# Performance work log

Hardware: AMD Instinct MI355X
Metric: run time of the kernel (lower is better)

## Reference

```python
import jax, jax.numpy as jnp
import numpy as np


def setup_inputs() -> dict:
    key = jax.random.key(0)
    k1, k2, k3, k4 = jax.random.split(key, 4)
    B, H, W = 16, 256, 256
    CF = 128  # FeatureDA channels
    return {
        "infeat": jax.random.normal(k1, (B, 2, H, W), jnp.float32),
        "labelTpesudo": jax.random.uniform(k2, (B, 1, H, W), jnp.float32),
        "labelT": jax.random.uniform(k3, (B, 1, H, W), jnp.float32),
        "FeatureDA": jax.random.normal(k4, (B, CF, H, W), jnp.float32),
        "k": 2,
        "size": 32,
    }


def _gather_points(x, bi, yy, xx):
    # x: [B, C, H, W]; bi/yy/xx: [n_cls, B, k] -> [n_cls, B, k, C]
    return x.transpose(0, 2, 3, 1)[bi, yy, xx]


def reference(infeat, labelTpesudo, labelT, FeatureDA, k, size):
    B, C, H, W = infeat.shape  # C = 2 classes
    maxc = H - 1  # orisize - 1
    out = jax.nn.softmax(infeat, axis=1)  # channel softmax (implicit dim=1 for 4D)
    flat = out.reshape(B, C, H * W)
    # torch.topk(k*size*size, sorted=True); only the first k entries are used
    vals, idx = jax.lax.top_k(flat, k * size * size)  # [B, C, k*size*size]
    idx_k = idx[:, :, :k].transpose(1, 0, 2)   # [C, B, k], class-major like the c-loop
    vals_k = vals[:, :, :k].transpose(1, 0, 2)  # [C, B, k]
    # grid_xy: x = flat_index % W, y = flat_index // W
    py = idx_k // W
    px = idx_k % W
    bi = jnp.broadcast_to(jnp.arange(B)[None, :, None], idx_k.shape)
    # each loop iteration gathers a single pixel at (oy[0], ox[0]) = (py, px)
    # (stride=1, padding=0 => max(0, px*1-0) == px)
    classiferT = _gather_points(infeat, bi, py, px).reshape(-1, C)                      # 'ClassiferT'
    patchFeatDA = _gather_points(FeatureDA, bi, py, px).reshape(-1, FeatureDA.shape[1])  # 'patchFeatDA'
    labelTTrue = _gather_points(labelT, bi, py, px).reshape(-1, labelT.shape[1])
    labelpesudo = _gather_points(labelTpesudo, bi, py, px).reshape(-1, labelTpesudo.shape[1])
    provalue = vals_k.reshape(-1, 1)  # values[i, :, j]
    # oxy = [[ox0, ox1], [oy0, oy1]] with hardcoded 32-pixel extent, clamped to orisize-1
    ox = jnp.stack([px, jnp.minimum(px + 32 - 1, maxc)], axis=-1)
    oy = jnp.stack([py, jnp.minimum(py + 32 - 1, maxc)], axis=-1)
    pointXY = jnp.stack([ox, oy], axis=-2).reshape(-1, 2, 2).astype(jnp.int32)
    # concatenation order matches Pixel_select_gen: all unchg (c=0) then chg (c=1)
    return classiferT, patchFeatDA, labelTTrue, labelpesudo, provalue, pointXY
```

## Files before the change

kernel.cpp:

```cpp
#include <hip/hip_runtime.h>
#include <math.h>

static constexpr int Bb   = 16;
static constexpr int Ww   = 256;
static constexpr int HWp  = 256 * 256;
static constexpr int CF   = 128;
static constexpr int Kk   = 2;
static constexpr int SEGS = 8;
static constexpr int SEGLEN = HWp / SEGS;

__device__ __forceinline__ bool better(float v1, int i1, float v2, int i2) {
    return (v1 > v2) || ((v1 == v2) && (i1 < i2));
}

__global__ __launch_bounds__(256) void top2_partial(
    const float* __restrict__ infeat, float* __restrict__ ws_v, int* __restrict__ ws_i)
{
    const int row = blockIdx.x;
    const int seg = blockIdx.y;
    const int b = row >> 1, c = row & 1;
    const float* x0p = infeat + (size_t)(b * 2 + 0) * HWp;
    const float* x1p = infeat + (size_t)(b * 2 + 1) * HWp;
    const int t = threadIdx.x;

    float v0 = -INFINITY, v1 = -INFINITY;
    int   i0 = 0x7fffffff, i1 = 0x7fffffff;

    const int base = seg * SEGLEN + t * 4;
    #pragma unroll
    for (int it = 0; it < SEGLEN / (256 * 4); ++it) {
        const int p = base + it * (256 * 4);
        const float4 a  = *(const float4*)(x0p + p);
        const float4 bb = *(const float4*)(x1p + p);
        const float ax[4] = {a.x, a.y, a.z, a.w};
        const float bx[4] = {bb.x, bb.y, bb.z, bb.w};
        #pragma unroll
        for (int e = 0; e < 4; ++e) {
            const float m  = fmaxf(ax[e], bx[e]);
            const float e0 = expf(ax[e] - m);
            const float e1 = expf(bx[e] - m);
            const float v  = (c == 0 ? e0 : e1) / (e0 + e1);
            const int p2 = p + e;
            if (better(v, p2, v0, i0)) { v1 = v0; i1 = i0; v0 = v; i0 = p2; }
            else if (better(v, p2, v1, i1)) { v1 = v; i1 = p2; }
        }
    }

    __shared__ float sv[256][2];
    __shared__ int   si[256][2];
    sv[t][0] = v0; sv[t][1] = v1; si[t][0] = i0; si[t][1] = i1;
    __syncthreads();
    for (int s = 128; s > 0; s >>= 1) {
        if (t < s) {
            float a0 = sv[t][0], a1 = sv[t][1];
            int  ia0 = si[t][0], ia1 = si[t][1];
            float b0 = sv[t + s][0], b1 = sv[t + s][1];
            int  ib0 = si[t + s][0], ib1 = si[t + s][1];
            float r0, r1; int j0, j1;
            if (better(a0, ia0, b0, ib0)) {
                r0 = a0; j0 = ia0;
                if (better(b0, ib0, a1, ia1)) { r1 = b0; j1 = ib0; } else { r1 = a1; j1 = ia1; }
            } else {
                r0 = b0; j0 = ib0;
                if (better(a0, ia0, b1, ib1)) { r1 = a0; j1 = ia0; } else { r1 = b1; j1 = ib1; }
            }
            sv[t][0] = r0; sv[t][1] = r1; si[t][0] = j0; si[t][1] = j1;
        }
        __syncthreads();
    }
    if (t < 2) {
        ws_v[(row * SEGS + seg) * 2 + t] = sv[0][t];
        ws_i[(row * SEGS + seg) * 2 + t] = si[0][t];
    }
}

__global__ __launch_bounds__(128) void gather_out(
    const float* __restrict__ infeat,
    const float* __restrict__ labelTpesudo,
    const float* __restrict__ labelT,
    const float* __restrict__ FeatureDA,
    const float* __restrict__ ws_v, const int* __restrict__ ws_i,
    float* __restrict__ out)
{
    const int pi = blockIdx.x;
    const int c  = pi / (Bb * Kk);
    const int b  = (pi / Kk) % Bb;
    const int j  = pi % Kk;
    const int row = b * 2 + c;

    __shared__ float s_val;
    __shared__ int   s_idx;
    if (threadIdx.x == 0) {
        float bv0 = -INFINITY, bv1 = -INFINITY;
        int   bi0 = 0x7fffffff, bi1 = 0x7fffffff;
        for (int s2 = 0; s2 < SEGS; ++s2) {
            #pragma unroll
            for (int e = 0; e < 2; ++e) {
                const float v = ws_v[(row * SEGS + s2) * 2 + e];
                const int   i = ws_i[(row * SEGS + s2) * 2 + e];
                if (better(v, i, bv0, bi0)) { bv1 = bv0; bi1 = bi0; bv0 = v; bi0 = i; }
                else if (better(v, i, bv1, bi1)) { bv1 = v; bi1 = i; }
            }
        }
        s_val = (j == 0) ? bv0 : bv1;
        s_idx = (j == 0) ? bi0 : bi1;
    }
    __syncthreads();

    const int   idx = s_idx;
    const float val = s_val;
    const int py = idx >> 8;
    const int px = idx & (Ww - 1);
    const int t = threadIdx.x;

    out[128 + pi * CF + t] = FeatureDA[((size_t)b * CF + t) * HWp + idx];
    if (t < 2) out[pi * 2 + t] = infeat[((size_t)b * 2 + t) * HWp + idx];
    if (t == 0) {
        out[8320 + pi] = labelT[(size_t)b * HWp + idx];
        out[8384 + pi] = labelTpesudo[(size_t)b * HWp + idx];
        out[8448 + pi] = val;
        out[8512 + pi * 4 + 0] = (float)px;
        out[8512 + pi * 4 + 1] = (float)min(px + 31, 255);
        out[8512 + pi * 4 + 2] = (float)py;
        out[8512 + pi * 4 + 3] = (float)min(py + 31, 255);
    }
}

extern "C" void kernel_launch(void* const* d_in, const int* in_sizes, int n_in,
                              void* d_out, int out_size, void* d_ws, size_t ws_size,
                              hipStream_t stream) {
    const float* infeat       = (const float*)d_in[0];
    const float* labelTpesudo = (const float*)d_in[1];
    const float* labelT       = (const float*)d_in[2];
    const float* FeatureDA    = (const float*)d_in[3];
    float* out = (float*)d_out;

    float* ws_v = (float*)d_ws;
    int*   ws_i = (int*)((char*)d_ws + 32 * SEGS * 2 * sizeof(float));

    dim3 g1(32, SEGS);
    top2_partial<<<g1, 256, 0, stream>>>(infeat, ws_v, ws_i);
    gather_out<<<64, 128, 0, stream>>>(infeat, labelTpesudo, labelT, FeatureDA,
                                       ws_v, ws_i, out);
}
```

Baseline: 17.98 us.

## Compute both class top-2s per block and reduce with wave shuffles

```diff
diff --git a/kernel.cpp b/kernel.cpp
--- a/kernel.cpp
+++ b/kernel.cpp
@@ -6,30 +6,47 @@
 static constexpr int HWp  = 256 * 256;
 static constexpr int CF   = 128;
 static constexpr int Kk   = 2;
-static constexpr int SEGS = 8;
+static constexpr int SEGS = 16;
 static constexpr int SEGLEN = HWp / SEGS;
+static constexpr int THREADS = 256;
 
 __device__ __forceinline__ bool better(float v1, int i1, float v2, int i2) {
     return (v1 > v2) || ((v1 == v2) && (i1 < i2));
 }
 
-__global__ __launch_bounds__(256) void top2_partial(
+__device__ __forceinline__ void upd(float v, int p,
+                                    float& v0, int& i0, float& v1, int& i1) {
+    if (better(v, p, v0, i0)) { v1 = v0; i1 = i0; v0 = v; i0 = p; }
+    else if (better(v, p, v1, i1)) { v1 = v; i1 = p; }
+}
+
+__device__ __forceinline__ void merge2(float& a0, int& ia0, float& a1, int& ia1,
+                                       float b0, int ib0, float b1, int ib1) {
+    if (better(b0, ib0, a0, ia0)) {
+        float na1; int nia1;
+        if (better(a0, ia0, b1, ib1)) { na1 = a0; nia1 = ia0; }
+        else                          { na1 = b1; nia1 = ib1; }
+        a0 = b0; ia0 = ib0; a1 = na1; ia1 = nia1;
+    } else if (better(b0, ib0, a1, ia1)) {
+        a1 = b0; ia1 = ib0;
+    }
+}
+
+__global__ __launch_bounds__(THREADS) void top2_partial(
     const float* __restrict__ infeat, float* __restrict__ ws_v, int* __restrict__ ws_i)
 {
-    const int row = blockIdx.x;
+    const int b   = blockIdx.x;
     const int seg = blockIdx.y;
-    const int b = row >> 1, c = row & 1;
-    const float* x0p = infeat + (size_t)(b * 2 + 0) * HWp;
-    const float* x1p = infeat + (size_t)(b * 2 + 1) * HWp;
-    const int t = threadIdx.x;
+    const int t   = threadIdx.x;
+    const float* x0p = infeat + ((size_t)b * 2 + 0) * HWp + seg * SEGLEN;
+    const float* x1p = infeat + ((size_t)b * 2 + 1) * HWp + seg * SEGLEN;
 
-    float v0 = -INFINITY, v1 = -INFINITY;
-    int   i0 = 0x7fffffff, i1 = 0x7fffffff;
+    float u0 = -INFINITY, u1 = -INFINITY;  int ui0 = 0x7fffffff, ui1 = 0x7fffffff;
+    float w0 = -INFINITY, w1 = -INFINITY;  int wi0 = 0x7fffffff, wi1 = 0x7fffffff;
 
-    const int base = seg * SEGLEN + t * 4;
     #pragma unroll
-    for (int it = 0; it < SEGLEN / (256 * 4); ++it) {
-        const int p = base + it * (256 * 4);
+    for (int it = 0; it < SEGLEN / (THREADS * 4); ++it) {
+        const int p = it * (THREADS * 4) + t * 4;
         const float4 a  = *(const float4*)(x0p + p);
         const float4 bb = *(const float4*)(x1p + p);
         const float ax[4] = {a.x, a.y, a.z, a.w};
@@ -39,38 +56,48 @@
             const float m  = fmaxf(ax[e], bx[e]);
             const float e0 = expf(ax[e] - m);
             const float e1 = expf(bx[e] - m);
-            const float v  = (c == 0 ? e0 : e1) / (e0 + e1);
-            const int p2 = p + e;
-            if (better(v, p2, v0, i0)) { v1 = v0; i1 = i0; v0 = v; i0 = p2; }
-            else if (better(v, p2, v1, i1)) { v1 = v; i1 = p2; }
+            const float s  = e0 + e1;
+            const float va = e0 / s;
+            const float vb = e1 / s;
+            const int gp = seg * SEGLEN + p + e;
+            upd(va, gp, u0, ui0, u1, ui1);
+            upd(vb, gp, w0, wi0, w1, wi1);
         }
     }
 
-    __shared__ float sv[256][2];
-    __shared__ int   si[256][2];
-    sv[t][0] = v0; sv[t][1] = v1; si[t][0] = i0; si[t][1] = i1;
+    #pragma unroll
+    for (int m = 1; m < 64; m <<= 1) {
+        float ou0 = __shfl_xor(u0, m), ou1 = __shfl_xor(u1, m);
+        int  oui0 = __shfl_xor(ui0, m), oui1 = __shfl_xor(ui1, m);
+        float ow0 = __shfl_xor(w0, m), ow1 = __shfl_xor(w1, m);
+        int  owi0 = __shfl_xor(wi0, m), owi1 = __shfl_xor(wi1, m);
+        merge2(u0, ui0, u1, ui1, ou0, oui0, ou1, oui1);
+        merge2(w0, wi0, w1, wi1, ow0, owi0, ow1, owi1);
+    }
+
+    __shared__ float sv[4][2][2];
+    __shared__ int   si[4][2][2];
+    const int wave = t >> 6;
+    if ((t & 63) == 0) {
+        sv[wave][0][0] = u0; sv[wave][0][1] = u1;
+        sv[wave][1][0] = w0; sv[wave][1][1] = w1;
+        si[wave][0][0] = ui0; si[wave][0][1] = ui1;
+        si[wave][1][0] = wi0; si[wave][1][1] = wi1;
+    }
     __syncthreads();
-    for (int s = 128; s > 0; s >>= 1) {
-        if (t < s) {
-            float a0 = sv[t][0], a1 = sv[t][1];
-            int  ia0 = si[t][0], ia1 = si[t][1];
-            float b0 = sv[t + s][0], b1 = sv[t + s][1];
-            int  ib0 = si[t + s][0], ib1 = si[t + s][1];
-            float r0, r1; int j0, j1;
-            if (better(a0, ia0, b0, ib0)) {
-                r0 = a0; j0 = ia0;
-                if (better(b0, ib0, a1, ia1)) { r1 = b0; j1 = ib0; } else { r1 = a1; j1 = ia1; }
-            } else {
-                r0 = b0; j0 = ib0;
-                if (better(a0, ia0, b1, ib1)) { r1 = a0; j1 = ia0; } else { r1 = b1; j1 = ib1; }
-            }
-            sv[t][0] = r0; sv[t][1] = r1; si[t][0] = j0; si[t][1] = j1;
+    if (t == 0) {
+        #pragma unroll
+        for (int wv = 1; wv < 4; ++wv) {
+            merge2(sv[0][0][0], si[0][0][0], sv[0][0][1], si[0][0][1],
+                   sv[wv][0][0], si[wv][0][0], sv[wv][0][1], si[wv][0][1]);
+            merge2(sv[0][1][0], si[0][1][0], sv[0][1][1], si[0][1][1],
+                   sv[wv][1][0], si[wv][1][0], sv[wv][1][1], si[wv][1][1]);
         }
-        __syncthreads();
-    }
-    if (t < 2) {
-        ws_v[(row * SEGS + seg) * 2 + t] = sv[0][t];
-        ws_i[(row * SEGS + seg) * 2 + t] = si[0][t];
+        const int base = ((b * SEGS + seg) * 2) * 2;
+        ws_v[base + 0] = sv[0][0][0]; ws_v[base + 1] = sv[0][0][1];
+        ws_v[base + 2] = sv[0][1][0]; ws_v[base + 3] = sv[0][1][1];
+        ws_i[base + 0] = si[0][0][0]; ws_i[base + 1] = si[0][0][1];
+        ws_i[base + 2] = si[0][1][0]; ws_i[base + 3] = si[0][1][1];
     }
 }
 
@@ -86,7 +113,6 @@
     const int c  = pi / (Bb * Kk);
     const int b  = (pi / Kk) % Bb;
     const int j  = pi % Kk;
-    const int row = b * 2 + c;
 
     __shared__ float s_val;
     __shared__ int   s_idx;
@@ -94,10 +120,11 @@
         float bv0 = -INFINITY, bv1 = -INFINITY;
         int   bi0 = 0x7fffffff, bi1 = 0x7fffffff;
         for (int s2 = 0; s2 < SEGS; ++s2) {
+            const int base = ((b * SEGS + s2) * 2 + c) * 2;
             #pragma unroll
             for (int e = 0; e < 2; ++e) {
-                const float v = ws_v[(row * SEGS + s2) * 2 + e];
-                const int   i = ws_i[(row * SEGS + s2) * 2 + e];
+                const float v = ws_v[base + e];
+                const int   i = ws_i[base + e];
                 if (better(v, i, bv0, bi0)) { bv1 = bv0; bi1 = bi0; bv0 = v; bi0 = i; }
                 else if (better(v, i, bv1, bi1)) { bv1 = v; bi1 = i; }
             }
@@ -136,10 +163,10 @@
     float* out = (float*)d_out;
 
     float* ws_v = (float*)d_ws;
-    int*   ws_i = (int*)((char*)d_ws + 32 * SEGS * 2 * sizeof(float));
+    int*   ws_i = (int*)((char*)d_ws + Bb * SEGS * 4 * sizeof(float));
 
-    dim3 g1(32, SEGS);
-    top2_partial<<<g1, 256, 0, stream>>>(infeat, ws_v, ws_i);
+    dim3 g1(Bb, SEGS);
+    top2_partial<<<g1, THREADS, 0, stream>>>(infeat, ws_v, ws_i);
     gather_out<<<64, 128, 0, stream>>>(infeat, labelTpesudo, labelT, FeatureDA,
                                        ws_v, ws_i, out);
 }
```

New measurement: 26.57 us. +47.8%, slower.
